# Kernel tuning notes

Hardware: AMD Instinct MI355X
Metric: run time of the kernel (lower is better)

The kernel has to match this reference:

```python
import jax, jax.numpy as jnp
import numpy as np
import math

B, S, HID = 2, 2048, 1024
NH, HD = 16, 64
MAX_SEQ = 65536  # RoPE base from RotaryEmbedding


def _rope_tables(seq_len, dim):
    inv_freq = 1.0 / (MAX_SEQ ** (jnp.arange(0, dim, 2, dtype=jnp.float32) / dim))
    t = jnp.arange(seq_len, dtype=jnp.float32)
    freqs = jnp.einsum('i,j->ij', t, inv_freq)          # [S, dim/2]
    emb = jnp.concatenate([freqs, freqs], axis=-1)      # [S, dim]
    return jnp.cos(emb), jnp.sin(emb)


def _rotate_half(x):
    x1, x2 = jnp.split(x, 2, axis=-1)
    return jnp.concatenate([-x2, x1], axis=-1)


def setup_inputs() -> dict:
    key = jax.random.key(0)
    ks = jax.random.split(key, 9)
    std_qkv = 1.0 / math.sqrt(NH * HD)
    std_o = 1.0 / math.sqrt(HID)
    return {
        'input_embeds': jax.random.normal(ks[0], (B, S, HID), dtype=jnp.float32),
        'Wq': jax.random.normal(ks[1], (NH * HD, HID), dtype=jnp.float32) * std_qkv,
        'bq': jnp.zeros((NH * HD,), dtype=jnp.float32),
        'Wk': jax.random.normal(ks[2], (NH * HD, HID), dtype=jnp.float32) * std_qkv,
        'bk': jnp.zeros((NH * HD,), dtype=jnp.float32),
        'Wv': jax.random.normal(ks[3], (NH * HD, HID), dtype=jnp.float32) * std_qkv,
        'bv': jnp.zeros((NH * HD,), dtype=jnp.float32),
        'Wo': jax.random.normal(ks[4], (HID, NH * HD), dtype=jnp.float32) * std_o,
        'bo': jnp.zeros((HID,), dtype=jnp.float32),
    }


def reference(input_embeds, Wq, bq, Wk, bk, Wv, bv, Wo, bo):
    x = input_embeds
    b, s, _ = x.shape
    # QKV projections (torch Linear: x @ W.T + b)
    q = x @ Wq.T + bq
    k = x @ Wk.T + bk
    v = x @ Wv.T + bv
    # [B, S, NH*HD] -> [B, NH, S, HD]
    q = q.reshape(b, s, NH, HD).transpose(0, 2, 1, 3)
    k = k.reshape(b, s, NH, HD).transpose(0, 2, 1, 3)
    v = v.reshape(b, s, NH, HD).transpose(0, 2, 1, 3)
    # RoPE
    cos, sin = _rope_tables(s, HD)  # [S, HD]
    q = q * cos + _rotate_half(q) * sin
    k = k * cos + _rotate_half(k) * sin
    # SDPA (non-causal, no mask)
    scale = 1.0 / math.sqrt(HD)
    scores = jnp.einsum('bhqd,bhkd->bhqk', q, k) * scale
    attn = jax.nn.softmax(scores, axis=-1)
    out = jnp.einsum('bhqk,bhkd->bhqd', attn, v)
    # [B, NH, S, HD] -> [B, S, NH*HD]
    out = out.transpose(0, 2, 1, 3).reshape(b, s, NH * HD)
    return out @ Wo.T + bo
```

## Files before the change

kernel.cpp:

```cpp
#include <hip/hip_runtime.h>
#include <cstdint>
#include <cstddef>

#define S_LEN 2048
#define NHEAD 16
#define HDIM  64
#define HID_  1024

typedef short s8v  __attribute__((ext_vector_type(8)));
typedef short s4v  __attribute__((ext_vector_type(4)));
typedef float f4v  __attribute__((ext_vector_type(4)));
typedef float f16v __attribute__((ext_vector_type(16)));

__device__ __forceinline__ short f2b(float x) {
    union { float f; unsigned u; } a; a.f = x;
    unsigned r = a.u + 0x7fffu + ((a.u >> 16) & 1u);
    return (short)(r >> 16);
}
__device__ __forceinline__ float b2f(short x) {
    union { unsigned u; float f; } a; a.u = ((unsigned)(unsigned short)x) << 16;
    return a.f;
}

__device__ __forceinline__ unsigned cvtpk(float a, float b) {
    unsigned r;
    asm("v_cvt_pk_bf16_f32 %0, %1, %2" : "=v"(r) : "v"(a), "v"(b));
    return r;
}
__device__ __forceinline__ void plswap(unsigned& a, unsigned& b) {
    asm("v_permlane32_swap_b32 %0, %1" : "+v"(a), "+v"(b));
}

__global__ __launch_bounds__(256) void prep_kernel(
    const float* __restrict__ X,
    const float* __restrict__ Wq, const float* __restrict__ Wk,
    const float* __restrict__ Wv, const float* __restrict__ Wo,
    short* __restrict__ Xb, short* __restrict__ Wcat, short* __restrict__ Wob,
    float2* __restrict__ rtab)
{
    const int bid = blockIdx.x;
    if (bid < 8192) {
        const float* src;
        short* dst;
        int i;
        if (bid < 4096) {
            src = X; dst = Xb; i = bid * 256 + threadIdx.x;
        } else {
            int w = (bid - 4096) >> 10;
            src = (w == 0) ? Wq : (w == 1) ? Wk : (w == 2) ? Wv : Wo;
            dst = (w < 3) ? (Wcat + (size_t)w * 1048576) : Wob;
            i = ((bid - 4096) & 1023) * 256 + threadIdx.x;
        }
        float4 v = reinterpret_cast<const float4*>(src)[i];
        s4v o;
        o[0] = f2b(v.x); o[1] = f2b(v.y); o[2] = f2b(v.z); o[3] = f2b(v.w);
        reinterpret_cast<s4v*>(dst)[i] = o;
    } else {
        int idx = (bid - 8192) * 256 + threadIdx.x;
        int s = idx >> 5, j = idx & 31;
        float inv = exp2f(-0.5f * (float)j);
        float ang = (float)s * inv;
        float2 cs; cs.x = cosf(ang); cs.y = sinf(ang);
        rtab[idx] = cs;
    }
}

__global__ __launch_bounds__(256) void gemm_qkv(
    const short* __restrict__ A, const short* __restrict__ Bw,
    const float* __restrict__ bq, const float* __restrict__ bk,
    const float* __restrict__ bv,
    short* __restrict__ Qo, short* __restrict__ Ko, short* __restrict__ Vo,
    const float2* __restrict__ rtab)
{
    __shared__ short Asl[128 * 32];
    __shared__ short Bsl[128 * 32];
    const int t = threadIdx.x;
    const int lane = t & 63;
    const int l15 = lane & 15, l4 = lane >> 4;
    const int wid = t >> 6;
    const int blk = blockIdx.x;
    const int x = blk & 7, j = blk >> 3;
    const int tn = (x * 3 + j % 3) * 128;
    const int tm = (j / 3) * 128;
    const int K = 1024;
    const int wrow = (wid >> 1) * 64, wcol = (wid & 1) * 64;

    f4v acc[4][4];
#pragma unroll
    for (int i = 0; i < 4; ++i)
#pragma unroll
        for (int jj = 0; jj < 4; ++jj) acc[i][jj] = (f4v){0.f, 0.f, 0.f, 0.f};

    const int r0 = t >> 2;
    const int c0 = (t & 3) * 8;
    short* wA0 = Asl + t * 8;
    short* wA1 = Asl + 2048 * 8 / 8 * 8;
    (void)wA1;

    const short* Ap0 = A  + (size_t)(tm + r0)      * K + c0;
    const short* Ap1 = A  + (size_t)(tm + 64 + r0) * K + c0;
    const short* Bp0 = Bw + (size_t)(tn + r0)      * K + c0;
    const short* Bp1 = Bw + (size_t)(tn + 64 + r0) * K + c0;
    short* wAlo = Asl + t * 8;
    short* wAhi = Asl + 2048 + t * 8;
    short* wBlo = Bsl + t * 8;
    short* wBhi = Bsl + 2048 + t * 8;

    {
        s8v ga0 = *(const s8v*)(Ap0);
        s8v ga1 = *(const s8v*)(Ap1);
        s8v gb0 = *(const s8v*)(Bp0);
        s8v gb1 = *(const s8v*)(Bp1);
        *(s8v*)wAlo = ga0; *(s8v*)wAhi = ga1;
        *(s8v*)wBlo = gb0; *(s8v*)wBhi = gb1;
    }
    __syncthreads();

    for (int kt = 0; kt < 32; ++kt) {
        s8v ga0, ga1, gb0, gb1;
        const bool pre = (kt < 31);
        if (pre) {
            const int k0 = (kt + 1) << 5;
            ga0 = *(const s8v*)(Ap0 + k0);
            ga1 = *(const s8v*)(Ap1 + k0);
            gb0 = *(const s8v*)(Bp0 + k0);
            gb1 = *(const s8v*)(Bp1 + k0);
        }
        s8v af[4], bf[4];
#pragma unroll
        for (int i = 0; i < 4; ++i) {
            af[i] = *(const s8v*)&Asl[(wrow + i * 16 + l15) * 32 + 8 * l4];
            bf[i] = *(const s8v*)&Bsl[(wcol + i * 16 + l15) * 32 + 8 * l4];
        }
#pragma unroll
        for (int i = 0; i < 4; ++i)
#pragma unroll
            for (int jj = 0; jj < 4; ++jj)
                acc[i][jj] = __builtin_amdgcn_mfma_f32_16x16x32_bf16(af[i], bf[jj], acc[i][jj], 0, 0, 0);
        __syncthreads();
        if (pre) {
            *(s8v*)wAlo = ga0; *(s8v*)wAhi = ga1;
            *(s8v*)wBlo = gb0; *(s8v*)wBhi = gb1;
        }
        __syncthreads();
    }

    const int mode = tn >> 10;
    const float* bias = (mode == 0) ? bq : (mode == 1) ? bk : bv;
    short* outb = (mode == 0) ? Qo : (mode == 1) ? Ko : Vo;

    if (mode == 2) {
#pragma unroll
        for (int i = 0; i < 4; ++i) {
            int rowb = tm + wrow + i * 16 + l4 * 4;
            int b_ = rowb >> 11, s0 = rowb & 2047;
#pragma unroll
            for (int jj = 0; jj < 4; ++jj) {
                int col = tn + wcol + jj * 16 + l15;
                int cm = col & 1023;
                float bvv = bias[cm];
                int h = cm >> 6, d = col & 63;
                s4v o4;
#pragma unroll
                for (int r = 0; r < 4; ++r) o4[r] = f2b(acc[i][jj][r] + bvv);
                *(s4v*)&outb[((size_t)((b_ * NHEAD + h) * 64 + d)) * S_LEN + s0] = o4;
            }
        }
    } else {
        int h = ((tn & 1023) + wcol) >> 6;
        const float osc = (mode == 0) ? 0.180336880111f : 1.0f;
#pragma unroll
        for (int i = 0; i < 4; ++i) {
#pragma unroll
            for (int r = 0; r < 4; ++r) {
                int row = tm + wrow + i * 16 + l4 * 4 + r;
                int b_ = row >> 11, s = row & 2047;
                float2 cs0 = rtab[(s << 5) + l15];
                float2 cs1 = rtab[(s << 5) + 16 + l15];
#pragma unroll
                for (int jj = 0; jj < 4; ++jj) {
                    int col = tn + wcol + jj * 16 + l15;
                    int cm = col & 1023;
                    int d = col & 63;
                    float v  = acc[i][jj][r]     + bias[cm];
                    float vp = acc[i][jj ^ 2][r] + bias[cm ^ 32];
                    float2 cs = (jj & 1) ? cs1 : cs0;
                    float res = (d < 32) ? (v * cs.x - vp * cs.y)
                                         : (v * cs.x + vp * cs.y);
                    outb[(((size_t)(b_ * NHEAD + h) * S_LEN + s) << 6) + d] = f2b(res * osc);
                }
            }
        }
    }
}

__device__ __forceinline__ void gload_lds16(const void* g, void* l) {
    __builtin_amdgcn_global_load_lds(
        (__attribute__((address_space(1))) void*)const_cast<void*>(g),
        (__attribute__((address_space(3))) void*)l, 16, 0, 0);
}

__global__ __launch_bounds__(256) void gemm_o(
    const short* __restrict__ A, const short* __restrict__ Bw,
    const float* __restrict__ bias, float* __restrict__ outf)
{
    __shared__ short Asl[2][64 * 32];
    __shared__ short Bsl[2][128 * 32];
    const int t = threadIdx.x;
    const int lane = t & 63;
    const int l15 = lane & 15, l4 = lane >> 4;
    const int wid = t >> 6;
    const int blk = blockIdx.x;
    const int tn = (blk & 7) * 128;
    const int tm = (blk >> 3) * 64;
    const int K = 1024, N = 1024;
    const int wrow = (wid >> 1) * 32, wcol = (wid & 1) * 64;

    f4v acc[2][4];
#pragma unroll
    for (int i = 0; i < 2; ++i)
#pragma unroll
        for (int jj = 0; jj < 4; ++jj) acc[i][jj] = (f4v){0.f, 0.f, 0.f, 0.f};

    const int r0 = t >> 2;
    const int c0 = (t & 3) * 8;
    const int wbase = (t & ~63) * 8;

#define OSTAGE(buf, kt) do { const int k0_ = (kt) << 5;                            \
        gload_lds16(A  + (size_t)(tm + r0)      * K + k0_ + c0, &Asl[buf][wbase]);        \
        gload_lds16(Bw + (size_t)(tn + r0)      * K + k0_ + c0, &Bsl[buf][wbase]);        \
        gload_lds16(Bw + (size_t)(tn + 64 + r0) * K + k0_ + c0, &Bsl[buf][2048 + wbase]); \
    } while (0)

    OSTAGE(0, 0);
    int cur = 0;
    for (int kt = 0; kt < 32; ++kt) {
        if (kt < 31) {
            OSTAGE(cur ^ 1, kt + 1);
            asm volatile("s_waitcnt vmcnt(3)" ::: "memory");
        } else {
            asm volatile("s_waitcnt vmcnt(0)" ::: "memory");
        }
        __builtin_amdgcn_s_barrier();
        __builtin_amdgcn_sched_barrier(0);
        s8v af[2], bf[4];
#pragma unroll
        for (int i = 0; i < 2; ++i)
            af[i] = *(const s8v*)&Asl[cur][(wrow + i * 16 + l15) * 32 + 8 * l4];
#pragma unroll
        for (int jj = 0; jj < 4; ++jj)
            bf[jj] = *(const s8v*)&Bsl[cur][(wcol + jj * 16 + l15) * 32 + 8 * l4];
#pragma unroll
        for (int i = 0; i < 2; ++i)
#pragma unroll
            for (int jj = 0; jj < 4; ++jj)
                acc[i][jj] = __builtin_amdgcn_mfma_f32_16x16x32_bf16(af[i], bf[jj], acc[i][jj], 0, 0, 0);
        __builtin_amdgcn_s_barrier();
        cur ^= 1;
    }
#undef OSTAGE

#pragma unroll
    for (int i = 0; i < 2; ++i) {
        int rowb = tm + wrow + i * 16 + l4 * 4;
#pragma unroll
        for (int jj = 0; jj < 4; ++jj) {
            int col = tn + wcol + jj * 16 + l15;
            float bv = bias[col];
#pragma unroll
            for (int r = 0; r < 4; ++r)
                outf[(size_t)(rowb + r) * N + col] = acc[i][jj][r] + bv;
        }
    }
}

#define SWB(row, bofs) ((bofs) ^ (((row) & 7) << 4))

__global__ __launch_bounds__(512) void attn_split(
    const short* __restrict__ Q, const short* __restrict__ K,
    const short* __restrict__ Vt,
    short* __restrict__ P0, short* __restrict__ P1, float2* __restrict__ ML)
{
    __shared__ short Kl[4096];
    __shared__ short Vl[4096];

    const int t = threadIdx.x, lane = t & 63;
    const int wid = t >> 6;
    const int q5 = lane & 31, hi = lane >> 5;

    const int blk = blockIdx.x;
    const int x = blk & 7, j = blk >> 3;
    const int bh = x * 4 + (j & 3);
    const int rest = j >> 2;
    const int qb = rest & 7, split = rest >> 3;
    const int kt0 = split * 16;

    const short* Qb = Q + (size_t)bh * S_LEN * 64;
    const char*  Kb = (const char*)(K  + (size_t)bh * S_LEN * 64);
    const char*  Vb = (const char*)(Vt + (size_t)bh * S_LEN * 64);
    const int qrow = qb * 256 + wid * 32 + q5;

    s8v qf[4];
#pragma unroll
    for (int sl = 0; sl < 4; ++sl)
        qf[sl] = *(const s8v*)&Qb[(size_t)qrow * 64 + sl * 16 + hi * 8];

    f16v oacc[2];
#pragma unroll
    for (int dt = 0; dt < 2; ++dt)
#pragma unroll
        for (int e = 0; e < 16; ++e) oacc[dt][e] = 0.f;
    float m2 = -1e30f, lsum = 0.f;

    const int skey  = t >> 3;
    const int sboff = (t & 7) * 16;
    const int sw    = SWB(skey, sboff);
    const size_t kgoff = (size_t)skey * 128  + sboff;
    const size_t vgoff = (size_t)skey * 4096 + sboff;
    char* KlB = (char*)Kl;
    char* VlB = (char*)Vl;
    const int w0 = skey * 128 + sw;

    {
        const size_t kbB = (size_t)kt0 * 64 * 128;
        const size_t vbB = (size_t)kt0 * 64 * 2;
        s8v g0 = *(const s8v*)(Kb + kbB + kgoff);
        s8v g1 = *(const s8v*)(Vb + vbB + vgoff);
        *(s8v*)(KlB + w0) = g0;
        *(s8v*)(VlB + w0) = g1;
    }
    __syncthreads();

    for (int kt = kt0; kt < kt0 + 16; ++kt) {
        s8v g0, g1;
        const bool pre = (kt < kt0 + 15);
        if (pre) {
            const size_t kbB = (size_t)(kt + 1) * 64 * 128;
            const size_t vbB = (size_t)(kt + 1) * 64 * 2;
            g0 = *(const s8v*)(Kb + kbB + kgoff);
            g1 = *(const s8v*)(Vb + vbB + vgoff);
        }

        f16v sc[2];
#pragma unroll
        for (int e = 0; e < 16; ++e) { sc[0][e] = 0.f; sc[1][e] = 0.f; }
        {
            const int kr0 = q5, kr1 = 32 + q5;
            const char* kb0 = KlB + kr0 * 128;
            const char* kb1 = KlB + kr1 * 128;
            __builtin_amdgcn_s_setprio(1);
#pragma unroll
            for (int sl = 0; sl < 4; ++sl) {
                s8v kf0 = *(const s8v*)(kb0 + SWB(kr0, sl * 32 + hi * 16));
                s8v kf1 = *(const s8v*)(kb1 + SWB(kr1, sl * 32 + hi * 16));
                sc[0] = __builtin_amdgcn_mfma_f32_32x32x16_bf16(kf0, qf[sl], sc[0], 0, 0, 0);
                sc[1] = __builtin_amdgcn_mfma_f32_32x32x16_bf16(kf1, qf[sl], sc[1], 0, 0, 0);
            }
            __builtin_amdgcn_s_setprio(0);
        }

        float m8[8];
#pragma unroll
        for (int e = 0; e < 8; ++e)
            m8[e] = fmaxf(fmaxf(sc[0][e], sc[0][e + 8]), fmaxf(sc[1][e], sc[1][e + 8]));
        float pm = fmaxf(fmaxf(fmaxf(m8[0], m8[4]), fmaxf(m8[1], m8[5])),
                         fmaxf(fmaxf(m8[2], m8[6]), fmaxf(m8[3], m8[7])));
        pm = fmaxf(pm, __shfl_xor(pm, 32, 64));
        if (__any(pm > m2 + 8.0f)) {
            float m2n = fmaxf(m2, pm);
            float fr = __builtin_amdgcn_exp2f(m2 - m2n);
            lsum *= fr;
#pragma unroll
            for (int dt = 0; dt < 2; ++dt)
#pragma unroll
                for (int e = 0; e < 16; ++e) oacc[dt][e] *= fr;
            m2 = m2n;
        }
#pragma unroll
        for (int c = 0; c < 2; ++c)
#pragma unroll
            for (int e = 0; e < 16; ++e)
                sc[c][e] = __builtin_amdgcn_exp2f(sc[c][e] - m2);
        float sum8[8];
#pragma unroll
        for (int e = 0; e < 8; ++e)
            sum8[e] = (sc[0][e] + sc[0][e + 8]) + (sc[1][e] + sc[1][e + 8]);
        lsum += ((sum8[0] + sum8[4]) + (sum8[1] + sum8[5])) +
                ((sum8[2] + sum8[6]) + (sum8[3] + sum8[7]));

#pragma unroll
        for (int c = 0; c < 2; ++c) {
#pragma unroll
            for (int ks = 0; ks < 2; ++ks) {
                const int b0 = ks * 8;
                unsigned x0 = cvtpk(sc[c][b0 + 0], sc[c][b0 + 1]);
                unsigned y0 = cvtpk(sc[c][b0 + 4], sc[c][b0 + 5]);
                unsigned x1 = cvtpk(sc[c][b0 + 2], sc[c][b0 + 3]);
                unsigned y1 = cvtpk(sc[c][b0 + 6], sc[c][b0 + 7]);
                plswap(x0, y0);
                plswap(x1, y1);
                union { unsigned u[4]; s8v s; } pf;
                pf.u[0] = x0; pf.u[1] = x1; pf.u[2] = y0; pf.u[3] = y1;
                __builtin_amdgcn_s_setprio(1);
#pragma unroll
                for (int dt = 0; dt < 2; ++dt) {
                    const int vrow = dt * 32 + q5;
                    s8v vf = *(const s8v*)(VlB + vrow * 128 +
                                           SWB(vrow, c * 64 + ks * 32 + hi * 16));
                    oacc[dt] = __builtin_amdgcn_mfma_f32_32x32x16_bf16(vf, pf.s, oacc[dt], 0, 0, 0);
                }
                __builtin_amdgcn_s_setprio(0);
            }
        }

        __syncthreads();
        if (pre) {
            *(s8v*)(KlB + w0) = g0;
            *(s8v*)(VlB + w0) = g1;
        }
        __syncthreads();
    }

    float ls = lsum + __shfl_xor(lsum, 32, 64);
    float inv = 1.0f / ls;
    short* Pp = (split ? P1 : P0) + ((size_t)bh * S_LEN + qrow) * 64;
#pragma unroll
    for (int dt = 0; dt < 2; ++dt)
#pragma unroll
        for (int g = 0; g < 4; ++g) {
            s4v o4;
#pragma unroll
            for (int jj = 0; jj < 4; ++jj) o4[jj] = f2b(oacc[dt][g * 4 + jj] * inv);
            const int d0 = dt * 32 + g * 8 + hi * 4;
            *(s4v*)&Pp[d0] = o4;
        }
    if (hi == 0) {
        float2 ml; ml.x = m2; ml.y = ls;
        ML[(size_t)split * (32 * S_LEN) + bh * S_LEN + qrow] = ml;
    }
}

__global__ __launch_bounds__(256) void attn_combine(
    const short* __restrict__ P0, const short* __restrict__ P1,
    const float2* __restrict__ ML, short* __restrict__ Obf)
{
    int idx = blockIdx.x * 256 + threadIdx.x;
    int row = idx >> 3;
    int d0 = (idx & 7) * 8;
    float2 a = ML[row];
    float2 b = ML[32 * S_LEN + row];
    float m = fmaxf(a.x, b.x);
    float w0 = a.y * exp2f(a.x - m);
    float w1 = b.y * exp2f(b.x - m);
    float inv = 1.0f / (w0 + w1);
    w0 *= inv; w1 *= inv;
    s8v v0 = *(const s8v*)&P0[(size_t)row * 64 + d0];
    s8v v1 = *(const s8v*)&P1[(size_t)row * 64 + d0];
    s8v o;
#pragma unroll
    for (int e = 0; e < 8; ++e) o[e] = f2b(w0 * b2f(v0[e]) + w1 * b2f(v1[e]));
    int bh = row >> 11, s = row & 2047;
    int b_ = bh >> 4, h = bh & 15;
    *(s8v*)&Obf[((size_t)(b_ * S_LEN + s)) * HID_ + h * 64 + d0] = o;
}

extern "C" void kernel_launch(void* const* d_in, const int* in_sizes, int n_in,
                              void* d_out, int out_size, void* d_ws, size_t ws_size,
                              hipStream_t stream)
{
    const float* X  = (const float*)d_in[0];
    const float* Wq = (const float*)d_in[1];
    const float* bq = (const float*)d_in[2];
    const float* Wk = (const float*)d_in[3];
    const float* bk = (const float*)d_in[4];
    const float* Wv = (const float*)d_in[5];
    const float* bv = (const float*)d_in[6];
    const float* Wo = (const float*)d_in[7];
    const float* bo = (const float*)d_in[8];
    float* out = (float*)d_out;

    char* ws = (char*)d_ws;
    short*  Xb   = (short*) (ws);
    short*  Wcat = (short*) (ws + ( 8u << 20));
    short*  Wob  = (short*) (ws + (14u << 20));
    float2* rtab = (float2*)(ws + (16u << 20));
    short*  Qbh  = (short*) (ws + (17u << 20));
    short*  Kbh  = (short*) (ws + (25u << 20));
    short*  Vbh  = (short*) (ws + (33u << 20));
    short*  Obf  = (short*) (ws + (41u << 20));
    short*  P0   = (short*) (ws);
    short*  P1   = (short*) d_out;
    float2* ML   = (float2*)((char*)d_out + (8u << 20));

    prep_kernel<<<8448, 256, 0, stream>>>(X, Wq, Wk, Wv, Wo, Xb, Wcat, Wob, rtab);
    gemm_qkv<<<768, 256, 0, stream>>>(Xb, Wcat, bq, bk, bv, Qbh, Kbh, Vbh, rtab);
    attn_split<<<512, 512, 0, stream>>>(Qbh, Kbh, Vbh, P0, P1, ML);
    attn_combine<<<2048, 256, 0, stream>>>(P0, P1, ML, Obf);
    gemm_o<<<512, 256, 0, stream>>>(Obf, Wob, bo, out);
}
```

Measured before the change: 146.4 us.

## Read K/V fragments directly from global memory in attention, dropping LDS staging

```diff
diff --git a/kernel.cpp b/kernel.cpp
--- a/kernel.cpp
+++ b/kernel.cpp
@@ -93,9 +93,6 @@
 
     const int r0 = t >> 2;
     const int c0 = (t & 3) * 8;
-    short* wA0 = Asl + t * 8;
-    short* wA1 = Asl + 2048 * 8 / 8 * 8;
-    (void)wA1;
 
     const short* Ap0 = A  + (size_t)(tm + r0)      * K + c0;
     const short* Ap1 = A  + (size_t)(tm + 64 + r0) * K + c0;
@@ -274,16 +271,11 @@
     }
 }
 
-#define SWB(row, bofs) ((bofs) ^ (((row) & 7) << 4))
-
-__global__ __launch_bounds__(512) void attn_split(
+__global__ __launch_bounds__(256, 4) void attn_split(
     const short* __restrict__ Q, const short* __restrict__ K,
     const short* __restrict__ Vt,
     short* __restrict__ P0, short* __restrict__ P1, float2* __restrict__ ML)
 {
-    __shared__ short Kl[4096];
-    __shared__ short Vl[4096];
-
     const int t = threadIdx.x, lane = t & 63;
     const int wid = t >> 6;
     const int q5 = lane & 31, hi = lane >> 5;
@@ -292,13 +284,13 @@
     const int x = blk & 7, j = blk >> 3;
     const int bh = x * 4 + (j & 3);
     const int rest = j >> 2;
-    const int qb = rest & 7, split = rest >> 3;
+    const int qb = rest & 15, split = rest >> 4;
     const int kt0 = split * 16;
 
     const short* Qb = Q + (size_t)bh * S_LEN * 64;
     const char*  Kb = (const char*)(K  + (size_t)bh * S_LEN * 64);
     const char*  Vb = (const char*)(Vt + (size_t)bh * S_LEN * 64);
-    const int qrow = qb * 256 + wid * 32 + q5;
+    const int qrow = qb * 128 + wid * 32 + q5;
 
     s8v qf[4];
 #pragma unroll
@@ -312,47 +304,25 @@
         for (int e = 0; e < 16; ++e) oacc[dt][e] = 0.f;
     float m2 = -1e30f, lsum = 0.f;
 
-    const int skey  = t >> 3;
-    const int sboff = (t & 7) * 16;
-    const int sw    = SWB(skey, sboff);
-    const size_t kgoff = (size_t)skey * 128  + sboff;
-    const size_t vgoff = (size_t)skey * 4096 + sboff;
-    char* KlB = (char*)Kl;
-    char* VlB = (char*)Vl;
-    const int w0 = skey * 128 + sw;
-
-    {
-        const size_t kbB = (size_t)kt0 * 64 * 128;
-        const size_t vbB = (size_t)kt0 * 64 * 2;
-        s8v g0 = *(const s8v*)(Kb + kbB + kgoff);
-        s8v g1 = *(const s8v*)(Vb + vbB + vgoff);
-        *(s8v*)(KlB + w0) = g0;
-        *(s8v*)(VlB + w0) = g1;
-    }
-    __syncthreads();
+    const char* kr0base = Kb + (size_t)q5 * 128;
+    const char* kr1base = Kb + (size_t)(32 + q5) * 128;
+    const char* v0base  = Vb + (size_t)q5 * 4096;
+    const char* v1base  = Vb + (size_t)(32 + q5) * 4096;
+    const int hb = hi * 16;
 
     for (int kt = kt0; kt < kt0 + 16; ++kt) {
-        s8v g0, g1;
-        const bool pre = (kt < kt0 + 15);
-        if (pre) {
-            const size_t kbB = (size_t)(kt + 1) * 64 * 128;
-            const size_t vbB = (size_t)(kt + 1) * 64 * 2;
-            g0 = *(const s8v*)(Kb + kbB + kgoff);
-            g1 = *(const s8v*)(Vb + vbB + vgoff);
-        }
+        const size_t kcol = (size_t)kt * 64 * 128;
+        const size_t vcol = (size_t)kt * 128;
 
         f16v sc[2];
 #pragma unroll
         for (int e = 0; e < 16; ++e) { sc[0][e] = 0.f; sc[1][e] = 0.f; }
         {
-            const int kr0 = q5, kr1 = 32 + q5;
-            const char* kb0 = KlB + kr0 * 128;
-            const char* kb1 = KlB + kr1 * 128;
             __builtin_amdgcn_s_setprio(1);
 #pragma unroll
             for (int sl = 0; sl < 4; ++sl) {
-                s8v kf0 = *(const s8v*)(kb0 + SWB(kr0, sl * 32 + hi * 16));
-                s8v kf1 = *(const s8v*)(kb1 + SWB(kr1, sl * 32 + hi * 16));
+                s8v kf0 = *(const s8v*)(kr0base + kcol + sl * 32 + hb);
+                s8v kf1 = *(const s8v*)(kr1base + kcol + sl * 32 + hb);
                 sc[0] = __builtin_amdgcn_mfma_f32_32x32x16_bf16(kf0, qf[sl], sc[0], 0, 0, 0);
                 sc[1] = __builtin_amdgcn_mfma_f32_32x32x16_bf16(kf1, qf[sl], sc[1], 0, 0, 0);
             }
@@ -392,6 +362,9 @@
         for (int c = 0; c < 2; ++c) {
 #pragma unroll
             for (int ks = 0; ks < 2; ++ks) {
+                const size_t vo = vcol + c * 64 + ks * 32 + hb;
+                s8v vf0 = *(const s8v*)(v0base + vo);
+                s8v vf1 = *(const s8v*)(v1base + vo);
                 const int b0 = ks * 8;
                 unsigned x0 = cvtpk(sc[c][b0 + 0], sc[c][b0 + 1]);
                 unsigned y0 = cvtpk(sc[c][b0 + 4], sc[c][b0 + 5]);
@@ -402,23 +375,11 @@
                 union { unsigned u[4]; s8v s; } pf;
                 pf.u[0] = x0; pf.u[1] = x1; pf.u[2] = y0; pf.u[3] = y1;
                 __builtin_amdgcn_s_setprio(1);
-#pragma unroll
-                for (int dt = 0; dt < 2; ++dt) {
-                    const int vrow = dt * 32 + q5;
-                    s8v vf = *(const s8v*)(VlB + vrow * 128 +
-                                           SWB(vrow, c * 64 + ks * 32 + hi * 16));
-                    oacc[dt] = __builtin_amdgcn_mfma_f32_32x32x16_bf16(vf, pf.s, oacc[dt], 0, 0, 0);
-                }
+                oacc[0] = __builtin_amdgcn_mfma_f32_32x32x16_bf16(vf0, pf.s, oacc[0], 0, 0, 0);
+                oacc[1] = __builtin_amdgcn_mfma_f32_32x32x16_bf16(vf1, pf.s, oacc[1], 0, 0, 0);
                 __builtin_amdgcn_s_setprio(0);
             }
         }
-
-        __syncthreads();
-        if (pre) {
-            *(s8v*)(KlB + w0) = g0;
-            *(s8v*)(VlB + w0) = g1;
-        }
-        __syncthreads();
     }
 
     float ls = lsum + __shfl_xor(lsum, 32, 64);
@@ -494,7 +455,7 @@
 
     prep_kernel<<<8448, 256, 0, stream>>>(X, Wq, Wk, Wv, Wo, Xb, Wcat, Wob, rtab);
     gemm_qkv<<<768, 256, 0, stream>>>(Xb, Wcat, bq, bk, bv, Qbh, Kbh, Vbh, rtab);
-    attn_split<<<512, 512, 0, stream>>>(Qbh, Kbh, Vbh, P0, P1, ML);
+    attn_split<<<1024, 256, 0, stream>>>(Qbh, Kbh, Vbh, P0, P1, ML);
     attn_combine<<<2048, 256, 0, stream>>>(P0, P1, ML, Obf);
     gemm_o<<<512, 256, 0, stream>>>(Obf, Wob, bo, out);
 }
```

Result: slower. 210.5 us (+43.8%).
